# Performance work log

Measured on AMD Instinct MI355X. Metric: run time of the kernel, lower is better.

The kernel has to match this reference:

```python
import jax, jax.numpy as jnp
import numpy as np

LOG_CLAMP = -100.0  # torch BCE clamps log terms at -100


def _weights_from_target(target):
    # target: [B, 1, W, W]; weight[b,i,j] = W / (sqrt((i-x)^2 + (j-y)^2) + 1)
    # where (x, y) is the mean location of the per-sample max of target.
    B = target.shape[0]
    W = target.shape[-1]
    t = target.reshape(B, W, W)
    m = jnp.max(t, axis=(1, 2), keepdims=True)
    mask = (t == m).astype(t.dtype)                      # all argmax locations
    cnt = jnp.sum(mask, axis=(1, 2))                     # [B]
    idx = jnp.arange(W, dtype=t.dtype)
    x = jnp.sum(mask * idx[None, :, None], axis=(1, 2)) / cnt  # mean row index
    y = jnp.sum(mask * idx[None, None, :], axis=(1, 2)) / cnt  # mean col index
    a = idx[None, :, None] - x[:, None, None]            # [B, W, 1]
    b = idx[None, None, :] - y[:, None, None]            # [B, 1, W]
    dist = (jnp.sqrt(a * a + b * b) + 1.0) / W           # [B, W, W]
    return (1.0 / dist).reshape(target.shape)


def reference(input, target):
    weights = _weights_from_target(target)
    log_p = jnp.maximum(jnp.log(input), LOG_CLAMP)
    log_1mp = jnp.maximum(jnp.log1p(-input), LOG_CLAMP)
    bce = -(target * log_p + (1.0 - target) * log_1mp)
    return jnp.mean(weights * bce)


def setup_inputs() -> dict:
    key = jax.random.key(0)
    k1, k2 = jax.random.split(key)
    shape = (256, 1, 224, 224)
    # BCE requires probabilities in (0,1); keep strictly inside via small margin.
    input = jax.random.uniform(k1, shape, dtype=jnp.float32, minval=1e-4, maxval=1.0 - 1e-4)
    target = jax.random.uniform(k2, shape, dtype=jnp.float32)
    return {"input": input, "target": target}
```

## Files before the change

kernel.cpp:

```cpp
#include <hip/hip_runtime.h>
#include <hip/hip_fp16.h>
#include <math.h>


#define WIMG 224
#define WW (WIMG * WIMG)
#define NQ (WW / 4)
#define NB 256
#define NT 1024
#define NIT (NQ / NT)
#define REM (NQ - NIT * NT)
#define LDS_BYTES (2 * NQ * 4)
#define LN2 0.69314718055994530942f
#define CLAMP2 (-144.269504088896340736f)

__device__ __forceinline__ float bce2_elem(float p, float t)
{
    float lp2  = fmaxf(__builtin_amdgcn_logf(p),        CLAMP2);
    float l1p2 = fmaxf(__builtin_amdgcn_logf(1.0f - p), CLAMP2);
    return l1p2 + t * (lp2 - l1p2);
}

__global__ __launch_bounds__(NT) void floss_kernel(
    const float* __restrict__ input,
    const float* __restrict__ target,
    float* __restrict__ out,
    float inv_total)
{
    extern __shared__ __half2 bce_lds[];
    const int b   = blockIdx.x;
    const int tid = threadIdx.x;
    const float4* __restrict__ t4 = (const float4*)(target + (size_t)b * WW);
    const float4* __restrict__ p4 = (const float4*)(input  + (size_t)b * WW);

    const bool has_tail = tid < REM;
    const int qt = NIT * NT + tid;
    float4 tvt = {}, pvt = {};
    if (has_tail) { tvt = t4[qt]; pvt = p4[qt]; }

    float m = -1.0f, cnt = 0.0f, si = 0.0f, sj = 0.0f;
    float4 tva = t4[tid],      pva = p4[tid];
    float4 tvb = t4[NT + tid], pvb = p4[NT + tid];
    #pragma unroll
    for (int it = 0; it < NIT; ++it) {
        float4 tvn, pvn;
        if (it + 2 < NIT) { tvn = t4[(it + 2) * NT + tid]; pvn = p4[(it + 2) * NT + tid]; }
        float4 tv = tva, pv = pva;
        int q  = it * NT + tid;
        int i  = q / 56;
        int j0 = (q - i * 56) * 4;
        float fi = (float)i;

        float mq  = fmaxf(fmaxf(tv.x, tv.y), fmaxf(tv.z, tv.w));
        float cq  = (tv.x == mq ? 1.0f : 0.0f) + (tv.y == mq ? 1.0f : 0.0f)
                  + (tv.z == mq ? 1.0f : 0.0f) + (tv.w == mq ? 1.0f : 0.0f);
        float sjq = (tv.x == mq ? (float)(j0 + 0) : 0.0f)
                  + (tv.y == mq ? (float)(j0 + 1) : 0.0f)
                  + (tv.z == mq ? (float)(j0 + 2) : 0.0f)
                  + (tv.w == mq ? (float)(j0 + 3) : 0.0f);
        float siq = fi * cq;
        bool gt = mq > m, eq = mq == m;
        cnt = gt ? cq  : (cnt + (eq ? cq  : 0.0f));
        si  = gt ? siq : (si  + (eq ? siq : 0.0f));
        sj  = gt ? sjq : (sj  + (eq ? sjq : 0.0f));
        m   = fmaxf(m, mq);

        bce_lds[q]      = __floats2half2_rn(bce2_elem(pv.x, tv.x), bce2_elem(pv.y, tv.y));
        bce_lds[NQ + q] = __floats2half2_rn(bce2_elem(pv.z, tv.z), bce2_elem(pv.w, tv.w));

        tva = tvb; pva = pvb;
        tvb = tvn; pvb = pvn;
    }
    if (has_tail) {
        int q  = qt;
        int i  = q / 56;
        int j0 = (q - i * 56) * 4;
        float fi = (float)i;
        float4 tv = tvt, pv = pvt;
        float mq  = fmaxf(fmaxf(tv.x, tv.y), fmaxf(tv.z, tv.w));
        float cq  = (tv.x == mq ? 1.0f : 0.0f) + (tv.y == mq ? 1.0f : 0.0f)
                  + (tv.z == mq ? 1.0f : 0.0f) + (tv.w == mq ? 1.0f : 0.0f);
        float sjq = (tv.x == mq ? (float)(j0 + 0) : 0.0f)
                  + (tv.y == mq ? (float)(j0 + 1) : 0.0f)
                  + (tv.z == mq ? (float)(j0 + 2) : 0.0f)
                  + (tv.w == mq ? (float)(j0 + 3) : 0.0f);
        float siq = fi * cq;
        bool gt = mq > m, eq = mq == m;
        cnt = gt ? cq  : (cnt + (eq ? cq  : 0.0f));
        si  = gt ? siq : (si  + (eq ? siq : 0.0f));
        sj  = gt ? sjq : (sj  + (eq ? sjq : 0.0f));
        m   = fmaxf(m, mq);
        bce_lds[q]      = __floats2half2_rn(bce2_elem(pv.x, tv.x), bce2_elem(pv.y, tv.y));
        bce_lds[NQ + q] = __floats2half2_rn(bce2_elem(pv.z, tv.z), bce2_elem(pv.w, tv.w));
    }

    #pragma unroll
    for (int off = 32; off > 0; off >>= 1) {
        float m2  = __shfl_down(m,   off);
        float c2  = __shfl_down(cnt, off);
        float si2 = __shfl_down(si,  off);
        float sj2 = __shfl_down(sj,  off);
        bool gt = m2 > m, eq = m2 == m;
        cnt = gt ? c2  : (cnt + (eq ? c2  : 0.0f));
        si  = gt ? si2 : (si  + (eq ? si2 : 0.0f));
        sj  = gt ? sj2 : (sj  + (eq ? sj2 : 0.0f));
        m   = fmaxf(m, m2);
    }
    __shared__ float sm[16], sc[16], ssi[16], ssj[16];
    __shared__ float sxy[2];
    const int lane = tid & 63, wid = tid >> 6;
    if (lane == 0) { sm[wid] = m; sc[wid] = cnt; ssi[wid] = si; ssj[wid] = sj; }
    __syncthreads();
    if (tid == 0) {
        float M = sm[0], C = sc[0], SI = ssi[0], SJ = ssj[0];
        #pragma unroll
        for (int w = 1; w < 16; ++w) {
            float mw = sm[w];
            bool gt = mw > M, eq = mw == M;
            C  = gt ? sc[w]  : (C  + (eq ? sc[w]  : 0.0f));
            SI = gt ? ssi[w] : (SI + (eq ? ssi[w] : 0.0f));
            SJ = gt ? ssj[w] : (SJ + (eq ? ssj[w] : 0.0f));
            M  = fmaxf(M, mw);
        }
        sxy[0] = SI / C;
        sxy[1] = SJ / C;
    }
    __syncthreads();
    const float x = sxy[0], y = sxy[1];
    const float Kc = -(float)WIMG * LN2;

    float acc = 0.0f;
    #pragma unroll
    for (int it = 0; it <= NIT; ++it) {
        if (it == NIT && !has_tail) break;
        int q = (it < NIT) ? (it * NT + tid) : qt;
        float2 b01 = __half22float2(bce_lds[q]);
        float2 b23 = __half22float2(bce_lds[NQ + q]);
        int i  = q / 56;
        int j0 = (q - i * 56) * 4;
        float di  = (float)i - x;
        float di2 = di * di;
        float bb[4] = {b01.x, b01.y, b23.x, b23.y};
        #pragma unroll
        for (int k = 0; k < 4; ++k) {
            float dj = (float)(j0 + k) - y;
            float s  = __builtin_amdgcn_sqrtf(di2 + dj * dj);
            float wf = Kc * __builtin_amdgcn_rcpf(s + 1.0f);
            acc += wf * bb[k];
        }
    }

    #pragma unroll
    for (int off = 32; off > 0; off >>= 1) acc += __shfl_down(acc, off);
    __shared__ float sred[16];
    if (lane == 0) sred[wid] = acc;
    __syncthreads();
    if (tid == 0) {
        float ssum = 0.0f;
        #pragma unroll
        for (int w = 0; w < 16; ++w) ssum += sred[w];
        atomicAdd(out, ssum * inv_total);
    }
}

extern "C" void kernel_launch(void* const* d_in, const int* in_sizes, int n_in,
                              void* d_out, int out_size, void* d_ws, size_t ws_size,
                              hipStream_t stream) {
    const float* input  = (const float*)d_in[0];
    const float* target = (const float*)d_in[1];
    float* out = (float*)d_out;
    hipFuncSetAttribute((const void*)floss_kernel,
                        hipFuncAttributeMaxDynamicSharedMemorySize, LDS_BYTES);
    hipMemsetAsync(out, 0, sizeof(float), stream);
    const float inv_total = 1.0f / (256.0f * 224.0f * 224.0f);
    floss_kernel<<<NB, NT, LDS_BYTES, stream>>>(input, target, out, inv_total);
}
```

Baseline: 122.2 us.

## Stream inputs via global_load_lds double buffering and store BCE in fp8

Loads of target and input now go straight into LDS through global_load_lds into two staging buffers, with a barrier each iteration, replacing the register-prefetched float4 loads. The cached per-element BCE values are packed as fp8 instead of fp16, which halves their LDS footprint and leaves room for the staging buffers. The goal is to cut register pressure and improve load latency hiding. In exchange it adds a block-wide sync per iteration, and fp8 storage loses a lot of BCE precision, which may push the weighted mean outside tolerance.

```diff
diff --git a/kernel.cpp b/kernel.cpp
--- a/kernel.cpp
+++ b/kernel.cpp
@@ -1,5 +1,4 @@
 #include <hip/hip_runtime.h>
-#include <hip/hip_fp16.h>
 #include <math.h>
 
 
@@ -8,11 +7,15 @@
 #define NQ (WW / 4)
 #define NB 256
 #define NT 1024
-#define NIT (NQ / NT)
-#define REM (NQ - NIT * NT)
-#define LDS_BYTES (2 * NQ * 4)
+#define NIT 12
+#define REM 256
+#define STAGE_BYTES 32768
+#define BCE8_OFF 65536
+#define LDS_BYTES (BCE8_OFF + NQ * 4)
 #define LN2 0.69314718055994530942f
 #define CLAMP2 (-144.269504088896340736f)
+
+typedef float floatx2 __attribute__((ext_vector_type(2)));
 
 __device__ __forceinline__ float bce2_elem(float p, float t)
 {
@@ -27,25 +30,39 @@
     float* __restrict__ out,
     float inv_total)
 {
-    extern __shared__ __half2 bce_lds[];
+    extern __shared__ __align__(16) char lds[];
     const int b   = blockIdx.x;
     const int tid = threadIdx.x;
     const float4* __restrict__ t4 = (const float4*)(target + (size_t)b * WW);
     const float4* __restrict__ p4 = (const float4*)(input  + (size_t)b * WW);
+    const int woff = (tid >> 6) << 10;
+
+    auto issue = [&](int it, int buf) {
+        int q = it * NT + tid;
+        char* lt = lds + buf * STAGE_BYTES + woff;
+        char* lp = lds + buf * STAGE_BYTES + 16384 + woff;
+        __builtin_amdgcn_global_load_lds(
+            (const __attribute__((address_space(1))) void*)(t4 + q),
+            (__attribute__((address_space(3))) void*)lt, 16, 0, 0);
+        __builtin_amdgcn_global_load_lds(
+            (const __attribute__((address_space(1))) void*)(p4 + q),
+            (__attribute__((address_space(3))) void*)lp, 16, 0, 0);
+    };
 
     const bool has_tail = tid < REM;
     const int qt = NIT * NT + tid;
     float4 tvt = {}, pvt = {};
     if (has_tail) { tvt = t4[qt]; pvt = p4[qt]; }
+    issue(0, 0);
 
     float m = -1.0f, cnt = 0.0f, si = 0.0f, sj = 0.0f;
-    float4 tva = t4[tid],      pva = p4[tid];
-    float4 tvb = t4[NT + tid], pvb = p4[NT + tid];
     #pragma unroll
     for (int it = 0; it < NIT; ++it) {
-        float4 tvn, pvn;
-        if (it + 2 < NIT) { tvn = t4[(it + 2) * NT + tid]; pvn = p4[(it + 2) * NT + tid]; }
-        float4 tv = tva, pv = pva;
+        __syncthreads();
+        if (it + 1 < NIT) issue(it + 1, (it + 1) & 1);
+        const int buf = it & 1;
+        float4 tv = *(const float4*)(lds + buf * STAGE_BYTES + (tid << 4));
+        float4 pv = *(const float4*)(lds + buf * STAGE_BYTES + 16384 + (tid << 4));
         int q  = it * NT + tid;
         int i  = q / 56;
         int j0 = (q - i * 56) * 4;
@@ -65,18 +82,18 @@
         sj  = gt ? sjq : (sj  + (eq ? sjq : 0.0f));
         m   = fmaxf(m, mq);
 
-        bce_lds[q]      = __floats2half2_rn(bce2_elem(pv.x, tv.x), bce2_elem(pv.y, tv.y));
-        bce_lds[NQ + q] = __floats2half2_rn(bce2_elem(pv.z, tv.z), bce2_elem(pv.w, tv.w));
-
-        tva = tvb; pva = pvb;
-        tvb = tvn; pvb = pvn;
+        int packed = __builtin_amdgcn_cvt_pk_fp8_f32(
+                         bce2_elem(pv.x, tv.x), bce2_elem(pv.y, tv.y), 0, false);
+        packed     = __builtin_amdgcn_cvt_pk_fp8_f32(
+                         bce2_elem(pv.z, tv.z), bce2_elem(pv.w, tv.w), packed, true);
+        ((int*)(lds + BCE8_OFF))[q] = packed;
     }
     if (has_tail) {
+        float4 tv = tvt, pv = pvt;
         int q  = qt;
         int i  = q / 56;
         int j0 = (q - i * 56) * 4;
         float fi = (float)i;
-        float4 tv = tvt, pv = pvt;
         float mq  = fmaxf(fmaxf(tv.x, tv.y), fmaxf(tv.z, tv.w));
         float cq  = (tv.x == mq ? 1.0f : 0.0f) + (tv.y == mq ? 1.0f : 0.0f)
                   + (tv.z == mq ? 1.0f : 0.0f) + (tv.w == mq ? 1.0f : 0.0f);
@@ -90,8 +107,11 @@
         si  = gt ? siq : (si  + (eq ? siq : 0.0f));
         sj  = gt ? sjq : (sj  + (eq ? sjq : 0.0f));
         m   = fmaxf(m, mq);
-        bce_lds[q]      = __floats2half2_rn(bce2_elem(pv.x, tv.x), bce2_elem(pv.y, tv.y));
-        bce_lds[NQ + q] = __floats2half2_rn(bce2_elem(pv.z, tv.z), bce2_elem(pv.w, tv.w));
+        int packed = __builtin_amdgcn_cvt_pk_fp8_f32(
+                         bce2_elem(pv.x, tv.x), bce2_elem(pv.y, tv.y), 0, false);
+        packed     = __builtin_amdgcn_cvt_pk_fp8_f32(
+                         bce2_elem(pv.z, tv.z), bce2_elem(pv.w, tv.w), packed, true);
+        ((int*)(lds + BCE8_OFF))[q] = packed;
     }
 
     #pragma unroll
@@ -134,8 +154,9 @@
     for (int it = 0; it <= NIT; ++it) {
         if (it == NIT && !has_tail) break;
         int q = (it < NIT) ? (it * NT + tid) : qt;
-        float2 b01 = __half22float2(bce_lds[q]);
-        float2 b23 = __half22float2(bce_lds[NQ + q]);
+        int packed = ((const int*)(lds + BCE8_OFF))[q];
+        floatx2 b01 = __builtin_amdgcn_cvt_pk_f32_fp8(packed, false);
+        floatx2 b23 = __builtin_amdgcn_cvt_pk_f32_fp8(packed, true);
         int i  = q / 56;
         int j0 = (q - i * 56) * 4;
         float di  = (float)i - x;
```

Measured after the change: 125.7 us. 1.03x slower.

## Split loss into stats+BCE kernel and weighting kernel with fp8 workspace

Applied to the files above, without the earlier changes.

Replaces the single per-image 1024-thread kernel, which kept fp16 BCE values in LDS, with two kernels over 7 chunks per image (1792 blocks of 256 threads). The first computes per-chunk argmax stats and writes BCE values packed as fp8 to global workspace. The second merges the stats, then applies the distance weights and reduces. This raises parallelism and occupancy beyond 256 large blocks, at the cost of an extra launch, a global round trip of the packed BCE data, and lower BCE precision from fp8 quantization.

```diff
diff --git a/kernel.cpp b/kernel.cpp
--- a/kernel.cpp
+++ b/kernel.cpp
@@ -1,18 +1,20 @@
 #include <hip/hip_runtime.h>
-#include <hip/hip_fp16.h>
 #include <math.h>
 
 
 #define WIMG 224
 #define WW (WIMG * WIMG)
 #define NQ (WW / 4)
-#define NB 256
-#define NT 1024
-#define NIT (NQ / NT)
-#define REM (NQ - NIT * NT)
-#define LDS_BYTES (2 * NQ * 4)
+#define NIMG 256
+#define NCH 7
+#define QCH (NQ / NCH)
+#define NT 256
+#define NIT (QCH / NT)
+#define NBLK (NIMG * NCH)
 #define LN2 0.69314718055994530942f
 #define CLAMP2 (-144.269504088896340736f)
+
+typedef float floatx2 __attribute__((ext_vector_type(2)));
 
 __device__ __forceinline__ float bce2_elem(float p, float t)
 {
@@ -21,32 +23,34 @@
     return l1p2 + t * (lp2 - l1p2);
 }
 
-__global__ __launch_bounds__(NT) void floss_kernel(
-    const float* __restrict__ input,
-    const float* __restrict__ target,
-    float* __restrict__ out,
-    float inv_total)
+__global__ __launch_bounds__(NT)
+__attribute__((amdgpu_waves_per_eu(4, 4)))
+void k1_stats_bce(const float* __restrict__ input,
+                  const float* __restrict__ target,
+                  float4* __restrict__ stats,
+                  int* __restrict__ bce8)
 {
-    extern __shared__ __half2 bce_lds[];
-    const int b   = blockIdx.x;
+    const int blk = blockIdx.x;
+    const int img = blk / NCH;
+    const int ch  = blk - img * NCH;
     const int tid = threadIdx.x;
-    const float4* __restrict__ t4 = (const float4*)(target + (size_t)b * WW);
-    const float4* __restrict__ p4 = (const float4*)(input  + (size_t)b * WW);
+    const float4* __restrict__ t4 = (const float4*)(target + (size_t)img * WW);
+    const float4* __restrict__ p4 = (const float4*)(input  + (size_t)img * WW);
+    const int qbase = ch * QCH;
 
-    const bool has_tail = tid < REM;
-    const int qt = NIT * NT + tid;
-    float4 tvt = {}, pvt = {};
-    if (has_tail) { tvt = t4[qt]; pvt = p4[qt]; }
+    float4 tt[NIT], pp[NIT];
+    #pragma unroll
+    for (int it = 0; it < NIT; ++it) {
+        int q = qbase + it * NT + tid;
+        tt[it] = t4[q];
+        pp[it] = p4[q];
+    }
 
     float m = -1.0f, cnt = 0.0f, si = 0.0f, sj = 0.0f;
-    float4 tva = t4[tid],      pva = p4[tid];
-    float4 tvb = t4[NT + tid], pvb = p4[NT + tid];
     #pragma unroll
     for (int it = 0; it < NIT; ++it) {
-        float4 tvn, pvn;
-        if (it + 2 < NIT) { tvn = t4[(it + 2) * NT + tid]; pvn = p4[(it + 2) * NT + tid]; }
-        float4 tv = tva, pv = pva;
-        int q  = it * NT + tid;
+        int q  = qbase + it * NT + tid;
+        float4 tv = tt[it], pv = pp[it];
         int i  = q / 56;
         int j0 = (q - i * 56) * 4;
         float fi = (float)i;
@@ -65,33 +69,11 @@
         sj  = gt ? sjq : (sj  + (eq ? sjq : 0.0f));
         m   = fmaxf(m, mq);
 
-        bce_lds[q]      = __floats2half2_rn(bce2_elem(pv.x, tv.x), bce2_elem(pv.y, tv.y));
-        bce_lds[NQ + q] = __floats2half2_rn(bce2_elem(pv.z, tv.z), bce2_elem(pv.w, tv.w));
-
-        tva = tvb; pva = pvb;
-        tvb = tvn; pvb = pvn;
-    }
-    if (has_tail) {
-        int q  = qt;
-        int i  = q / 56;
-        int j0 = (q - i * 56) * 4;
-        float fi = (float)i;
-        float4 tv = tvt, pv = pvt;
-        float mq  = fmaxf(fmaxf(tv.x, tv.y), fmaxf(tv.z, tv.w));
-        float cq  = (tv.x == mq ? 1.0f : 0.0f) + (tv.y == mq ? 1.0f : 0.0f)
-                  + (tv.z == mq ? 1.0f : 0.0f) + (tv.w == mq ? 1.0f : 0.0f);
-        float sjq = (tv.x == mq ? (float)(j0 + 0) : 0.0f)
-                  + (tv.y == mq ? (float)(j0 + 1) : 0.0f)
-                  + (tv.z == mq ? (float)(j0 + 2) : 0.0f)
-                  + (tv.w == mq ? (float)(j0 + 3) : 0.0f);
-        float siq = fi * cq;
-        bool gt = mq > m, eq = mq == m;
-        cnt = gt ? cq  : (cnt + (eq ? cq  : 0.0f));
-        si  = gt ? siq : (si  + (eq ? siq : 0.0f));
-        sj  = gt ? sjq : (sj  + (eq ? sjq : 0.0f));
-        m   = fmaxf(m, mq);
-        bce_lds[q]      = __floats2half2_rn(bce2_elem(pv.x, tv.x), bce2_elem(pv.y, tv.y));
-        bce_lds[NQ + q] = __floats2half2_rn(bce2_elem(pv.z, tv.z), bce2_elem(pv.w, tv.w));
+        int packed = __builtin_amdgcn_cvt_pk_fp8_f32(
+                         bce2_elem(pv.x, tv.x), bce2_elem(pv.y, tv.y), 0, false);
+        packed     = __builtin_amdgcn_cvt_pk_fp8_f32(
+                         bce2_elem(pv.z, tv.z), bce2_elem(pv.w, tv.w), packed, true);
+        bce8[(size_t)img * NQ + q] = packed;
     }
 
     #pragma unroll
@@ -106,15 +88,14 @@
         sj  = gt ? sj2 : (sj  + (eq ? sj2 : 0.0f));
         m   = fmaxf(m, m2);
     }
-    __shared__ float sm[16], sc[16], ssi[16], ssj[16];
-    __shared__ float sxy[2];
+    __shared__ float sm[4], sc[4], ssi[4], ssj[4];
     const int lane = tid & 63, wid = tid >> 6;
     if (lane == 0) { sm[wid] = m; sc[wid] = cnt; ssi[wid] = si; ssj[wid] = sj; }
     __syncthreads();
     if (tid == 0) {
         float M = sm[0], C = sc[0], SI = ssi[0], SJ = ssj[0];
         #pragma unroll
-        for (int w = 1; w < 16; ++w) {
+        for (int w = 1; w < 4; ++w) {
             float mw = sm[w];
             bool gt = mw > M, eq = mw == M;
             C  = gt ? sc[w]  : (C  + (eq ? sc[w]  : 0.0f));
@@ -122,20 +103,43 @@
             SJ = gt ? ssj[w] : (SJ + (eq ? ssj[w] : 0.0f));
             M  = fmaxf(M, mw);
         }
-        sxy[0] = SI / C;
-        sxy[1] = SJ / C;
+        stats[blk] = make_float4(M, C, SI, SJ);
     }
-    __syncthreads();
-    const float x = sxy[0], y = sxy[1];
+}
+
+__global__ __launch_bounds__(NT)
+void k2_weight(const int* __restrict__ bce8,
+               const float4* __restrict__ stats,
+               float* __restrict__ out,
+               float inv_total)
+{
+    const int blk = blockIdx.x;
+    const int img = blk / NCH;
+    const int ch  = blk - img * NCH;
+    const int tid = threadIdx.x;
+
+    float4 s0 = stats[img * NCH];
+    float M = s0.x, C = s0.y, SI = s0.z, SJ = s0.w;
+    #pragma unroll
+    for (int t = 1; t < NCH; ++t) {
+        float4 s = stats[img * NCH + t];
+        bool gt = s.x > M, eq = s.x == M;
+        C  = gt ? s.y : (C  + (eq ? s.y : 0.0f));
+        SI = gt ? s.z : (SI + (eq ? s.z : 0.0f));
+        SJ = gt ? s.w : (SJ + (eq ? s.w : 0.0f));
+        M  = fmaxf(M, s.x);
+    }
+    const float x = SI / C;
+    const float y = SJ / C;
     const float Kc = -(float)WIMG * LN2;
 
     float acc = 0.0f;
     #pragma unroll
-    for (int it = 0; it <= NIT; ++it) {
-        if (it == NIT && !has_tail) break;
-        int q = (it < NIT) ? (it * NT + tid) : qt;
-        float2 b01 = __half22float2(bce_lds[q]);
-        float2 b23 = __half22float2(bce_lds[NQ + q]);
+    for (int it = 0; it < NIT; ++it) {
+        int q = ch * QCH + it * NT + tid;
+        int packed = bce8[(size_t)img * NQ + q];
+        floatx2 b01 = __builtin_amdgcn_cvt_pk_f32_fp8(packed, false);
+        floatx2 b23 = __builtin_amdgcn_cvt_pk_f32_fp8(packed, true);
         int i  = q / 56;
         int j0 = (q - i * 56) * 4;
         float di  = (float)i - x;
@@ -152,14 +156,12 @@
 
     #pragma unroll
     for (int off = 32; off > 0; off >>= 1) acc += __shfl_down(acc, off);
-    __shared__ float sred[16];
+    __shared__ float sred[4];
+    const int lane = tid & 63, wid = tid >> 6;
     if (lane == 0) sred[wid] = acc;
     __syncthreads();
     if (tid == 0) {
-        float ssum = 0.0f;
-        #pragma unroll
-        for (int w = 0; w < 16; ++w) ssum += sred[w];
-        atomicAdd(out, ssum * inv_total);
+        atomicAdd(out, (sred[0] + sred[1] + sred[2] + sred[3]) * inv_total);
     }
 }
 
@@ -169,9 +171,11 @@
     const float* input  = (const float*)d_in[0];
     const float* target = (const float*)d_in[1];
     float* out = (float*)d_out;
-    hipFuncSetAttribute((const void*)floss_kernel,
-                        hipFuncAttributeMaxDynamicSharedMemorySize, LDS_BYTES);
+    float4* stats = (float4*)d_ws;
+    int*    bce8  = (int*)((char*)d_ws + NBLK * 16);
+
     hipMemsetAsync(out, 0, sizeof(float), stream);
     const float inv_total = 1.0f / (256.0f * 224.0f * 224.0f);
-    floss_kernel<<<NB, NT, LDS_BYTES, stream>>>(input, target, out, inv_total);
+    k1_stats_bce<<<NBLK, NT, 0, stream>>>(input, target, stats, bce8);
+    k2_weight<<<NBLK, NT, 0, stream>>>(bce8, stats, out, inv_total);
 }
```

Result: slower. 145.5 us (+19.1%).
